# Kernel optimization log

Measured on AMD Instinct MI355X. Metric: run time of the kernel, lower is better.

Reference implementation:

```python
import jax, jax.numpy as jnp
import numpy as np

N = 50000       # nodes
E = 1_600_000   # edges (avg degree 32)
NFEAT = 256
NHID = 128
NCLASS = 128    # must equal NHID for the gated skip connection to type-check


def setup_inputs() -> dict:
    key = jax.random.key(0)
    ks = jax.random.split(key, 16)
    g = 0.02  # xavier gain used in the module
    inp = {
        "x": jax.random.normal(ks[0], (N, NFEAT), dtype=jnp.float32),
        "row": jax.random.randint(ks[1], (E,), 0, N, dtype=jnp.int32),
        "col": jax.random.randint(ks[2], (E,), 0, N, dtype=jnp.int32),
        # GatedSkipConnection params (shared across the three skip calls)
        "W_sc": jax.random.normal(ks[3], (NFEAT, NHID), dtype=jnp.float32) * 0.05,
        "W_ci": jax.random.normal(ks[4], (NHID, NHID), dtype=jnp.float32) * 0.05,
        "b_ci": jnp.zeros((NHID,), dtype=jnp.float32),
        "W_co": jax.random.normal(ks[5], (NHID, NHID), dtype=jnp.float32) * 0.05,
        "b_co": jnp.zeros((NHID,), dtype=jnp.float32),
        # GraphSAGE layer weights: [2*in, out], bias [1, out] (init to 0 per module)
        "W0": jax.random.normal(ks[6], (2 * NFEAT, NHID), dtype=jnp.float32) * g,
        "b0": jnp.zeros((1, NHID), dtype=jnp.float32),
        "W1": jax.random.normal(ks[7], (2 * NHID, NHID), dtype=jnp.float32) * g,
        "b1": jnp.zeros((1, NHID), dtype=jnp.float32),
        "W2": jax.random.normal(ks[8], (2 * NHID, NCLASS), dtype=jnp.float32) * g,
        "b2": jnp.zeros((1, NCLASS), dtype=jnp.float32),
        # fc0: Linear(nhid, nclass)
        "Wf": jax.random.normal(ks[9], (NHID, NCLASS), dtype=jnp.float32) * 0.05,
        "bf": jnp.zeros((NCLASS,), dtype=jnp.float32),
    }
    return inp


def _sage(x, row, col, inv_deg, W, b):
    # adj @ x : sum source features x[col] into destination rows `row`
    agg = jax.ops.segment_sum(x[col], row, num_segments=N)  # [N, d]
    agg = agg * inv_deg[:, None]                            # degree normalization
    support = jnp.concatenate([x, agg], axis=1)             # [N, 2d]
    return support @ W + b


def _gsc(in_x, out_x, W_sc, W_ci, b_ci, W_co, b_co):
    in_x = in_x @ W_sc if in_x.shape[1] != out_x.shape[1] else in_x
    z = jax.nn.sigmoid(in_x @ W_ci + b_ci + out_x @ W_co + b_co)
    return z * out_x + (1.0 - z) * in_x


def reference(x, row, col, W_sc, W_ci, b_ci, W_co, b_co,
              W0, b0, W1, b1, W2, b2, Wf, bf):
    deg = jax.ops.segment_sum(jnp.ones((E,), x.dtype), row, num_segments=N)
    inv_deg = 1.0 / jnp.maximum(deg, 1.0)  # guard isolated nodes

    residual = x
    o1 = _sage(x, row, col, inv_deg, W0, b0)
    o3 = jax.nn.relu(_gsc(residual, o1, W_sc, W_ci, b_ci, W_co, b_co))
    o4 = _sage(o3, row, col, inv_deg, W1, b1)
    o6 = jax.nn.relu(_gsc(residual, o4, W_sc, W_ci, b_ci, W_co, b_co))
    o7 = _sage(o6, row, col, inv_deg, W2, b2)
    o8 = _gsc(residual, o7, W_sc, W_ci, b_ci, W_co, b_co)
    return o8 @ Wf + bf
```

## Files before the change

### kernel.cpp

```cpp
#include <hip/hip_runtime.h>
#include <hip/hip_bf16.h>
#include <hip/hip_fp16.h>
#include <math.h>

#define NN 50000
#define EE 1600000
#define NFEAT 256
#define NHID 128
#define RNG 6250
#define NPASS 8
#define CPAD 16

typedef _Float16 f16;
typedef _Float16 f16x8 __attribute__((ext_vector_type(8)));
typedef _Float16 f16x4 __attribute__((ext_vector_type(4)));
typedef float f32x4 __attribute__((ext_vector_type(4)));

struct WPtrs {
    const float* s[10];
    f16* d[10];
};

__global__ __launch_bounds__(256) void k_prep(const float* __restrict__ x,
                                              f16* __restrict__ xh, int n4,
                                              int* __restrict__ cnt, int nz4,
                                              WPtrs wp, int wtotal,
                                              int zb0, int wb0, int wblocks) {
    int b = blockIdx.x;
    if (b < zb0) {
        int i = b * 256 + threadIdx.x;
        if (i < n4) {
            float4 v = reinterpret_cast<const float4*>(x)[i];
            f16x4 h = {(f16)v.x, (f16)v.y, (f16)v.z, (f16)v.w};
            reinterpret_cast<f16x4*>(xh)[i] = h;
        }
    } else if (b < wb0) {
        int i = (b - zb0) * 256 + threadIdx.x;
        if (i < nz4) reinterpret_cast<int4*>(cnt)[i] = make_int4(0, 0, 0, 0);
    } else {
        for (int idx = (b - wb0) * 256 + threadIdx.x; idx < wtotal;
             idx += wblocks * 256) {
            int wsel, rem, K;
            if (idx < 3 * 32768) { wsel = idx >> 15; rem = idx & 32767; K = 256; }
            else { int t = idx - 3 * 32768; wsel = 3 + (t >> 14); rem = t & 16383; K = 128; }
            int k = rem >> 7, c = rem & 127;
            wp.d[wsel][c * K + k] = (f16)wp.s[wsel][rem];
        }
    }
}

__global__ void k_slot(const int* __restrict__ row, int* __restrict__ cnt,
                       int* __restrict__ eslot, int e) {
    int i = blockIdx.x * 256 + threadIdx.x;
    if (i < e) eslot[i] = atomicAdd(&cnt[(size_t)row[i] * CPAD], 1);
}

__global__ void k_scan1(const int* __restrict__ cnt, int* __restrict__ bsum, int n) {
    __shared__ int s[256];
    int t = threadIdx.x;
    int i = blockIdx.x * 256 + t;
    s[t] = (i < n) ? cnt[(size_t)i * CPAD] : 0;
    __syncthreads();
    for (int off = 128; off > 0; off >>= 1) {
        if (t < off) s[t] += s[t + off];
        __syncthreads();
    }
    if (t == 0) bsum[blockIdx.x] = s[0];
}

__global__ void k_scan3(const int* __restrict__ cnt, const int* __restrict__ bsum,
                        int* __restrict__ rp, float* __restrict__ invd,
                        int n, int nb) {
    __shared__ int buf[2][256];
    __shared__ int bpre[2][256];
    int t = threadIdx.x;

    bpre[0][t] = (t < nb) ? bsum[t] : 0;
    __syncthreads();
    int bs = 0;
    for (int off = 1; off < 256; off <<= 1) {
        int v = bpre[bs][t];
        if (t >= off) v += bpre[bs][t - off];
        bpre[bs ^ 1][t] = v;
        bs ^= 1;
        __syncthreads();
    }
    int base = (blockIdx.x == 0) ? 0 : bpre[bs][blockIdx.x - 1];

    int i = blockIdx.x * 256 + t;
    int v = (i < n) ? cnt[(size_t)i * CPAD] : 0;
    buf[0][t] = v;
    __syncthreads();
    int sel = 0;
    for (int off = 1; off < 256; off <<= 1) {
        int x = buf[sel][t];
        if (t >= off) x += buf[sel][t - off];
        buf[sel ^ 1][t] = x;
        sel ^= 1;
        __syncthreads();
    }
    int incl = buf[sel][t];
    int excl = incl - v;
    if (i < n) {
        rp[i] = base + excl;
        invd[i] = 1.0f / fmaxf((float)v, 1.0f);
        if (i == n - 1) rp[n] = base + incl;
    }
}

__global__ void k_fill8(const int* __restrict__ row, const int* __restrict__ col,
                        const int* __restrict__ eslot, const int* __restrict__ rp,
                        int* __restrict__ ci, int e) {
    int i = blockIdx.x * 256 + threadIdx.x;
    if (i >= e) return;
    int r = row[i];
    int lo = blockIdx.y * RNG;
    if (r >= lo && r < lo + RNG) ci[rp[r] + eslot[i]] = col[i];
}

__global__ __launch_bounds__(256) void k_agg2h(const f16* __restrict__ P,
                                               const int* __restrict__ rp,
                                               const int* __restrict__ ci,
                                               const float* __restrict__ invd,
                                               const f16* __restrict__ T,
                                               f16* __restrict__ OUT, int n) {
    int node = blockIdx.x * 16 + (threadIdx.x >> 4);
    if (node >= n) return;
    int lane = threadIdx.x & 15;
    int s = rp[node], e = rp[node + 1];
    float acc[8];
#pragma unroll
    for (int q = 0; q < 8; ++q) acc[q] = 0.0f;
    int j = s;
    for (; j + 8 <= e; j += 8) {
        f16x8 v[8];
#pragma unroll
        for (int u = 0; u < 8; ++u)
            v[u] = *reinterpret_cast<const f16x8*>(P + (size_t)ci[j + u] * 128 + lane * 8);
#pragma unroll
        for (int q = 0; q < 8; ++q)
            acc[q] += (((float)v[0][q] + (float)v[1][q]) + ((float)v[2][q] + (float)v[3][q])) +
                      (((float)v[4][q] + (float)v[5][q]) + ((float)v[6][q] + (float)v[7][q]));
    }
    for (; j < e; ++j) {
        f16x8 v0 = *reinterpret_cast<const f16x8*>(P + (size_t)ci[j] * 128 + lane * 8);
#pragma unroll
        for (int q = 0; q < 8; ++q) acc[q] += (float)v0[q];
    }
    float scl = invd[node];
    f16x8 tv = *reinterpret_cast<const f16x8*>(T + (size_t)node * 128 + lane * 8);
    f16x8 o;
#pragma unroll
    for (int q = 0; q < 8; ++q) o[q] = (f16)((float)tv[q] + scl * acc[q]);
    *reinterpret_cast<f16x8*>(OUT + (size_t)node * 128 + lane * 8) = o;
}

#define LDSSTR 40

__device__ __forceinline__ void stage_A(const f16* __restrict__ A, f16* sA,
                                        int row0, int K, int kb, int tid, int n) {
    int r = tid >> 2, ch = tid & 3;
    int gr = row0 + r;
    uint4 v = make_uint4(0, 0, 0, 0);
    if (gr < n) v = *reinterpret_cast<const uint4*>(A + (size_t)gr * K + kb + ch * 8);
    *reinterpret_cast<uint4*>(sA + r * LDSSTR + ch * 8) = v;
}

__device__ __forceinline__ void stage_B(const f16* __restrict__ Wt, f16* sB,
                                        int K, int kb, int tid) {
#pragma unroll
    for (int i = 0; i < 2; ++i) {
        int idx = tid + i * 256;
        int c = idx >> 2, ch = idx & 3;
        uint4 v = *reinterpret_cast<const uint4*>(Wt + (size_t)c * K + kb + ch * 8);
        *reinterpret_cast<uint4*>(sB + c * LDSSTR + ch * 8) = v;
    }
}

template <int K, int NW, bool F32OUT>
__global__ __launch_bounds__(256) void k_mgemm(const f16* __restrict__ A,
                                               const f16* __restrict__ Wt0,
                                               const f16* __restrict__ Wt1,
                                               const f16* __restrict__ Wt2,
                                               const float* __restrict__ bias0,
                                               void* __restrict__ C0,
                                               void* __restrict__ C1,
                                               void* __restrict__ C2, int n) {
    __shared__ f16 sA[64 * LDSSTR];
    __shared__ f16 sB[128 * LDSSTR];

    const f16* Wt = Wt0;
    const float* bias = bias0;
    void* C = C0;
    if (NW > 1 && blockIdx.y == 1) { Wt = Wt1; bias = nullptr; C = C1; }
    if (NW > 2 && blockIdx.y == 2) { Wt = Wt2; bias = nullptr; C = C2; }

    const int tid = threadIdx.x;
    const int row0 = blockIdx.x * 64;
    const int wid = tid >> 6, l = tid & 63;
    const int wr = wid >> 1, wc = wid & 1;
    const int lr = l & 15, lk = (l >> 4) * 8;

    f32x4 acc[2][4];
#pragma unroll
    for (int m = 0; m < 2; ++m)
#pragma unroll
        for (int q = 0; q < 4; ++q) acc[m][q] = (f32x4){0.f, 0.f, 0.f, 0.f};

    for (int kt = 0; kt < K / 32; ++kt) {
        stage_A(A, sA, row0, K, kt * 32, tid, n);
        stage_B(Wt, sB, K, kt * 32, tid);
        __syncthreads();
        f16x8 aF[2], bF[4];
#pragma unroll
        for (int m = 0; m < 2; ++m)
            aF[m] = *reinterpret_cast<f16x8*>(sA + (wr * 32 + m * 16 + lr) * LDSSTR + lk);
#pragma unroll
        for (int q = 0; q < 4; ++q)
            bF[q] = *reinterpret_cast<f16x8*>(sB + (wc * 64 + q * 16 + lr) * LDSSTR + lk);
#pragma unroll
        for (int m = 0; m < 2; ++m)
#pragma unroll
            for (int q = 0; q < 4; ++q)
                acc[m][q] = __builtin_amdgcn_mfma_f32_16x16x32_f16(aF[m], bF[q],
                                                                   acc[m][q], 0, 0, 0);
        __syncthreads();
    }

    const int lr4 = (l >> 4) * 4;
#pragma unroll
    for (int m = 0; m < 2; ++m)
#pragma unroll
        for (int q = 0; q < 4; ++q) {
            int c = wc * 64 + q * 16 + (l & 15);
            float b = bias ? bias[c] : 0.0f;
#pragma unroll
            for (int reg = 0; reg < 4; ++reg) {
                int r = row0 + wr * 32 + m * 16 + lr4 + reg;
                if (r >= n) continue;
                float v = acc[m][q][reg] + b;
                if (F32OUT) ((float*)C)[(size_t)r * 128 + c] = v;
                else        ((f16*)C)[(size_t)r * 128 + c] = (f16)v;
            }
        }
}

template <int RELU>
__global__ __launch_bounds__(256) void k_ggemm(const f16* __restrict__ Asc,
                                               const f16* __restrict__ At0,
                                               const f16* __restrict__ Wci,
                                               const f16* __restrict__ Wco,
                                               const float* __restrict__ bci,
                                               const float* __restrict__ bco,
                                               f16* __restrict__ C, int n) {
    __shared__ f16 sA[64 * LDSSTR];
    __shared__ f16 sB[128 * LDSSTR];

    const int tid = threadIdx.x;
    const int row0 = blockIdx.x * 64;
    const int wid = tid >> 6, l = tid & 63;
    const int wr = wid >> 1, wc = wid & 1;
    const int lr = l & 15, lk = (l >> 4) * 8;

    f32x4 acc[2][4];
#pragma unroll
    for (int m = 0; m < 2; ++m)
#pragma unroll
        for (int q = 0; q < 4; ++q) acc[m][q] = (f32x4){0.f, 0.f, 0.f, 0.f};

    for (int kt = 0; kt < 8; ++kt) {
        const f16* A = (kt < 4) ? Asc : At0;
        const f16* Wt = (kt < 4) ? Wci : Wco;
        int kb = (kt & 3) * 32;
        stage_A(A, sA, row0, 128, kb, tid, n);
        stage_B(Wt, sB, 128, kb, tid);
        __syncthreads();
        f16x8 aF[2], bF[4];
#pragma unroll
        for (int m = 0; m < 2; ++m)
            aF[m] = *reinterpret_cast<f16x8*>(sA + (wr * 32 + m * 16 + lr) * LDSSTR + lk);
#pragma unroll
        for (int q = 0; q < 4; ++q)
            bF[q] = *reinterpret_cast<f16x8*>(sB + (wc * 64 + q * 16 + lr) * LDSSTR + lk);
#pragma unroll
        for (int m = 0; m < 2; ++m)
#pragma unroll
            for (int q = 0; q < 4; ++q)
                acc[m][q] = __builtin_amdgcn_mfma_f32_16x16x32_f16(aF[m], bF[q],
                                                                   acc[m][q], 0, 0, 0);
        __syncthreads();
    }

    const int lr4 = (l >> 4) * 4;
#pragma unroll
    for (int m = 0; m < 2; ++m)
#pragma unroll
        for (int q = 0; q < 4; ++q) {
            int c = wc * 64 + q * 16 + (l & 15);
            float b = bci[c] + bco[c];
#pragma unroll
            for (int reg = 0; reg < 4; ++reg) {
                int r = row0 + wr * 32 + m * 16 + lr4 + reg;
                if (r >= n) continue;
                float v = acc[m][q][reg] + b;
                float z = 1.0f / (1.0f + __expf(-v));
                float o = (float)At0[(size_t)r * 128 + c];
                float s = (float)Asc[(size_t)r * 128 + c];
                float outv = z * o + (1.0f - z) * s;
                if (RELU) outv = fmaxf(outv, 0.0f);
                C[(size_t)r * 128 + c] = (f16)outv;
            }
        }
}

extern "C" void kernel_launch(void* const* d_in, const int* in_sizes, int n_in,
                              void* d_out, int out_size, void* d_ws, size_t ws_size,
                              hipStream_t stream) {
    const float* x    = (const float*)d_in[0];
    const int*   row  = (const int*)d_in[1];
    const int*   col  = (const int*)d_in[2];
    const float* W_sc = (const float*)d_in[3];
    const float* W_ci = (const float*)d_in[4];
    const float* b_ci = (const float*)d_in[5];
    const float* W_co = (const float*)d_in[6];
    const float* b_co = (const float*)d_in[7];
    const float* W0   = (const float*)d_in[8];
    const float* b0   = (const float*)d_in[9];
    const float* W1   = (const float*)d_in[10];
    const float* b1   = (const float*)d_in[11];
    const float* W2   = (const float*)d_in[12];
    const float* b2   = (const float*)d_in[13];
    const float* Wf   = (const float*)d_in[14];
    const float* bf   = (const float*)d_in[15];
    float* out = (float*)d_out;

    char* p = (char*)d_ws;
    auto alloc = [&](size_t bytes) {
        char* q = p;
        p += (bytes + 255) & ~(size_t)255;
        return q;
    };
    int*   cnt   = (int*)alloc((size_t)NN * CPAD * 4);
    int*   rp    = (int*)alloc((NN + 1) * 4);
    int*   bsum  = (int*)alloc(256 * 4);
    float* invd  = (float*)alloc(NN * 4);
    int*   ci    = (int*)alloc(EE * 4);
    int*   eslot = (int*)alloc(EE * 4);
    f16*   x_h   = (f16*)alloc((size_t)NN * 256 * 2);
    f16*   sc_h  = (f16*)alloc((size_t)NN * 128 * 2);
    f16*   T_h   = (f16*)alloc((size_t)NN * 128 * 2);
    f16*   P_h   = (f16*)alloc((size_t)NN * 128 * 2);
    f16*   t0_h  = (f16*)alloc((size_t)NN * 128 * 2);
    f16*   t1_h  = (f16*)alloc((size_t)NN * 128 * 2);
    f16* W0t_t = (f16*)alloc(256 * 128 * 2);
    f16* W0b_t = (f16*)alloc(256 * 128 * 2);
    f16* Wsc_t = (f16*)alloc(256 * 128 * 2);
    f16* W1t_t = (f16*)alloc(128 * 128 * 2);
    f16* W1b_t = (f16*)alloc(128 * 128 * 2);
    f16* W2t_t = (f16*)alloc(128 * 128 * 2);
    f16* W2b_t = (f16*)alloc(128 * 128 * 2);
    f16* Wci_t = (f16*)alloc(128 * 128 * 2);
    f16* Wco_t = (f16*)alloc(128 * 128 * 2);
    f16* Wf_t  = (f16*)alloc(128 * 128 * 2);

    const int NB_N  = (NN + 255) / 256;
    const int NB_E  = (EE + 255) / 256;
    const int GB    = (NN + 63) / 64;
    const int AGG_B = (NN + 15) / 16;

    const int N4   = NN * 256 / 4;
    const int NZ4  = NN * CPAD / 4;
    const int ZB0  = (N4 + 255) / 256;
    const int WB0  = ZB0 + (NZ4 + 255) / 256;
    const int WBLK = 84;
    const int WTOT = 3 * 32768 + 7 * 16384;
    WPtrs wp;
    wp.s[0] = W0;             wp.d[0] = W0t_t;
    wp.s[1] = W0 + 256 * 128; wp.d[1] = W0b_t;
    wp.s[2] = W_sc;           wp.d[2] = Wsc_t;
    wp.s[3] = W1;             wp.d[3] = W1t_t;
    wp.s[4] = W1 + 128 * 128; wp.d[4] = W1b_t;
    wp.s[5] = W2;             wp.d[5] = W2t_t;
    wp.s[6] = W2 + 128 * 128; wp.d[6] = W2b_t;
    wp.s[7] = W_ci;           wp.d[7] = Wci_t;
    wp.s[8] = W_co;           wp.d[8] = Wco_t;
    wp.s[9] = Wf;             wp.d[9] = Wf_t;
    k_prep<<<WB0 + WBLK, 256, 0, stream>>>(x, x_h, N4, cnt, NZ4, wp, WTOT,
                                           ZB0, WB0, WBLK);

    k_slot<<<NB_E, 256, 0, stream>>>(row, cnt, eslot, EE);
    k_scan1<<<NB_N, 256, 0, stream>>>(cnt, bsum, NN);
    k_scan3<<<NB_N, 256, 0, stream>>>(cnt, bsum, rp, invd, NN, NB_N);
    k_fill8<<<dim3(NB_E, NPASS), 256, 0, stream>>>(row, col, eslot, rp, ci, EE);

    k_mgemm<256, 3, false><<<dim3(GB, 3), 256, 0, stream>>>(
        x_h, W0t_t, W0b_t, Wsc_t, b0, T_h, P_h, sc_h, NN);
    k_agg2h<<<AGG_B, 256, 0, stream>>>(P_h, rp, ci, invd, T_h, t0_h, NN);
    k_ggemm<1><<<GB, 256, 0, stream>>>(sc_h, t0_h, Wci_t, Wco_t,
                                       b_ci, b_co, t1_h, NN);

    k_mgemm<128, 2, false><<<dim3(GB, 2), 256, 0, stream>>>(
        t1_h, W1t_t, W1b_t, nullptr, b1, T_h, P_h, nullptr, NN);
    k_agg2h<<<AGG_B, 256, 0, stream>>>(P_h, rp, ci, invd, T_h, t0_h, NN);
    k_ggemm<1><<<GB, 256, 0, stream>>>(sc_h, t0_h, Wci_t, Wco_t,
                                       b_ci, b_co, t1_h, NN);

    k_mgemm<128, 2, false><<<dim3(GB, 2), 256, 0, stream>>>(
        t1_h, W2t_t, W2b_t, nullptr, b2, T_h, P_h, nullptr, NN);
    k_agg2h<<<AGG_B, 256, 0, stream>>>(P_h, rp, ci, invd, T_h, t0_h, NN);
    k_ggemm<0><<<GB, 256, 0, stream>>>(sc_h, t0_h, Wci_t, Wco_t,
                                       b_ci, b_co, t1_h, NN);

    k_mgemm<128, 1, true><<<GB, 256, 0, stream>>>(
        t1_h, Wf_t, nullptr, nullptr, bf, out, nullptr, nullptr, NN);
}
```

Measured before the change: 541.8 us.

## Fuse gated skip with following SAGE GEMM, pack edge slot with row

Merges the gated-skip GEMM+sigmoid blend with the next layer's T/P projection GEMM (or the final classifier) into one kernel. The intermediate activation stays in LDS instead of going through global memory, and three launches are removed. Weights are read straight from global/L2 rather than staged in LDS. Edge slot and row are packed into one int, which assumes slot < 32768 and row < 65536, and the fill runs in 4 row-range passes instead of 8.

```diff
diff --git a/kernel.cpp b/kernel.cpp
--- a/kernel.cpp
+++ b/kernel.cpp
@@ -7,8 +7,8 @@
 #define EE 1600000
 #define NFEAT 256
 #define NHID 128
-#define RNG 6250
-#define NPASS 8
+#define RNG 12500
+#define NPASS 4
 #define CPAD 16
 
 typedef _Float16 f16;
@@ -50,9 +50,13 @@
 }
 
 __global__ void k_slot(const int* __restrict__ row, int* __restrict__ cnt,
-                       int* __restrict__ eslot, int e) {
+                       int* __restrict__ epack, int e) {
     int i = blockIdx.x * 256 + threadIdx.x;
-    if (i < e) eslot[i] = atomicAdd(&cnt[(size_t)row[i] * CPAD], 1);
+    if (i < e) {
+        int r = row[i];
+        int s = atomicAdd(&cnt[(size_t)r * CPAD], 1);
+        epack[i] = (s << 16) | r;
+    }
 }
 
 __global__ void k_scan1(const int* __restrict__ cnt, int* __restrict__ bsum, int n) {
@@ -108,14 +112,14 @@
     }
 }
 
-__global__ void k_fill8(const int* __restrict__ row, const int* __restrict__ col,
-                        const int* __restrict__ eslot, const int* __restrict__ rp,
-                        int* __restrict__ ci, int e) {
+__global__ void k_fill(const int* __restrict__ epack, const int* __restrict__ col,
+                       const int* __restrict__ rp, int* __restrict__ ci, int e) {
     int i = blockIdx.x * 256 + threadIdx.x;
     if (i >= e) return;
-    int r = row[i];
+    int pk = epack[i];
+    int r = pk & 0xFFFF;
     int lo = blockIdx.y * RNG;
-    if (r >= lo && r < lo + RNG) ci[rp[r] + eslot[i]] = col[i];
+    if (r >= lo && r < lo + RNG) ci[rp[r] + (pk >> 16)] = col[i];
 }
 
 __global__ __launch_bounds__(256) void k_agg2h(const f16* __restrict__ P,
@@ -245,70 +249,150 @@
         }
 }
 
-template <int RELU>
-__global__ __launch_bounds__(256) void k_ggemm(const f16* __restrict__ Asc,
+#define FSTR 136
+
+template <int RELU, bool CLS>
+__global__ __launch_bounds__(256) void k_fused(const f16* __restrict__ Asc,
                                                const f16* __restrict__ At0,
                                                const f16* __restrict__ Wci,
                                                const f16* __restrict__ Wco,
+                                               const f16* __restrict__ WtT,
+                                               const f16* __restrict__ WtP,
                                                const float* __restrict__ bci,
                                                const float* __restrict__ bco,
-                                               f16* __restrict__ C, int n) {
-    __shared__ f16 sA[64 * LDSSTR];
-    __shared__ f16 sB[128 * LDSSTR];
+                                               const float* __restrict__ bias2,
+                                               f16* __restrict__ To,
+                                               f16* __restrict__ Po,
+                                               float* __restrict__ Fo, int n) {
+    __shared__ f16 lsc[64 * FSTR];
+    __shared__ f16 lt0[64 * FSTR];
+    __shared__ f16 lt1[64 * FSTR];
 
     const int tid = threadIdx.x;
     const int row0 = blockIdx.x * 64;
     const int wid = tid >> 6, l = tid & 63;
     const int wr = wid >> 1, wc = wid & 1;
     const int lr = l & 15, lk = (l >> 4) * 8;
-
-    f32x4 acc[2][4];
-#pragma unroll
-    for (int m = 0; m < 2; ++m)
-#pragma unroll
-        for (int q = 0; q < 4; ++q) acc[m][q] = (f32x4){0.f, 0.f, 0.f, 0.f};
-
-    for (int kt = 0; kt < 8; ++kt) {
-        const f16* A = (kt < 4) ? Asc : At0;
-        const f16* Wt = (kt < 4) ? Wci : Wco;
-        int kb = (kt & 3) * 32;
-        stage_A(A, sA, row0, 128, kb, tid, n);
-        stage_B(Wt, sB, 128, kb, tid);
-        __syncthreads();
-        f16x8 aF[2], bF[4];
+    const int lr4 = (l >> 4) * 4;
+
+#pragma unroll
+    for (int i = 0; i < 4; ++i) {
+        int idx = tid + i * 256;
+        int r = idx >> 4, ch = idx & 15;
+        int gr = row0 + r;
+        uint4 vs = make_uint4(0, 0, 0, 0), vt = make_uint4(0, 0, 0, 0);
+        if (gr < n) {
+            vs = *reinterpret_cast<const uint4*>(Asc + (size_t)gr * 128 + ch * 8);
+            vt = *reinterpret_cast<const uint4*>(At0 + (size_t)gr * 128 + ch * 8);
+        }
+        *reinterpret_cast<uint4*>(lsc + r * FSTR + ch * 8) = vs;
+        *reinterpret_cast<uint4*>(lt0 + r * FSTR + ch * 8) = vt;
+    }
+    __syncthreads();
+
+    f32x4 accG[2][4];
+#pragma unroll
+    for (int m = 0; m < 2; ++m)
+#pragma unroll
+        for (int q = 0; q < 4; ++q) accG[m][q] = (f32x4){0.f, 0.f, 0.f, 0.f};
+
+#pragma unroll
+    for (int kt = 0; kt < 4; ++kt) {
+        f16x8 aS[2], aT[2], bC[4], bO[4];
+#pragma unroll
+        for (int m = 0; m < 2; ++m) {
+            int rr = (wr * 32 + m * 16 + lr) * FSTR + kt * 32 + lk;
+            aS[m] = *reinterpret_cast<const f16x8*>(lsc + rr);
+            aT[m] = *reinterpret_cast<const f16x8*>(lt0 + rr);
+        }
+#pragma unroll
+        for (int q = 0; q < 4; ++q) {
+            int c = wc * 64 + q * 16 + lr;
+            bC[q] = *reinterpret_cast<const f16x8*>(Wci + (size_t)c * 128 + kt * 32 + lk);
+            bO[q] = *reinterpret_cast<const f16x8*>(Wco + (size_t)c * 128 + kt * 32 + lk);
+        }
 #pragma unroll
         for (int m = 0; m < 2; ++m)
-            aF[m] = *reinterpret_cast<f16x8*>(sA + (wr * 32 + m * 16 + lr) * LDSSTR + lk);
-#pragma unroll
-        for (int q = 0; q < 4; ++q)
-            bF[q] = *reinterpret_cast<f16x8*>(sB + (wc * 64 + q * 16 + lr) * LDSSTR + lk);
+#pragma unroll
+            for (int q = 0; q < 4; ++q) {
+                accG[m][q] = __builtin_amdgcn_mfma_f32_16x16x32_f16(aS[m], bC[q],
+                                                                    accG[m][q], 0, 0, 0);
+                accG[m][q] = __builtin_amdgcn_mfma_f32_16x16x32_f16(aT[m], bO[q],
+                                                                    accG[m][q], 0, 0, 0);
+            }
+    }
+
+#pragma unroll
+    for (int m = 0; m < 2; ++m)
+#pragma unroll
+        for (int q = 0; q < 4; ++q) {
+            int c = wc * 64 + q * 16 + (l & 15);
+            float bb = bci[c] + bco[c];
+#pragma unroll
+            for (int reg = 0; reg < 4; ++reg) {
+                int lrow = wr * 32 + m * 16 + lr4 + reg;
+                float v = accG[m][q][reg] + bb;
+                float z = 1.0f / (1.0f + __expf(-v));
+                float o = (float)lt0[lrow * FSTR + c];
+                float s = (float)lsc[lrow * FSTR + c];
+                float t1v = z * o + (1.0f - z) * s;
+                if (RELU) t1v = fmaxf(t1v, 0.0f);
+                lt1[lrow * FSTR + c] = (f16)t1v;
+            }
+        }
+    __syncthreads();
+
+    f32x4 accT[2][4], accP[2][4];
+#pragma unroll
+    for (int m = 0; m < 2; ++m)
+#pragma unroll
+        for (int q = 0; q < 4; ++q) {
+            accT[m][q] = (f32x4){0.f, 0.f, 0.f, 0.f};
+            accP[m][q] = (f32x4){0.f, 0.f, 0.f, 0.f};
+        }
+
+#pragma unroll
+    for (int kt = 0; kt < 4; ++kt) {
+        f16x8 aF[2], bT[4], bP[4];
 #pragma unroll
         for (int m = 0; m < 2; ++m)
-#pragma unroll
-            for (int q = 0; q < 4; ++q)
-                acc[m][q] = __builtin_amdgcn_mfma_f32_16x16x32_f16(aF[m], bF[q],
-                                                                   acc[m][q], 0, 0, 0);
-        __syncthreads();
-    }
-
-    const int lr4 = (l >> 4) * 4;
+            aF[m] = *reinterpret_cast<const f16x8*>(
+                lt1 + (wr * 32 + m * 16 + lr) * FSTR + kt * 32 + lk);
+#pragma unroll
+        for (int q = 0; q < 4; ++q) {
+            int c = wc * 64 + q * 16 + lr;
+            bT[q] = *reinterpret_cast<const f16x8*>(WtT + (size_t)c * 128 + kt * 32 + lk);
+            if (!CLS)
+                bP[q] = *reinterpret_cast<const f16x8*>(WtP + (size_t)c * 128 + kt * 32 + lk);
+        }
+#pragma unroll
+        for (int m = 0; m < 2; ++m)
+#pragma unroll
+            for (int q = 0; q < 4; ++q) {
+                accT[m][q] = __builtin_amdgcn_mfma_f32_16x16x32_f16(aF[m], bT[q],
+                                                                    accT[m][q], 0, 0, 0);
+                if (!CLS)
+                    accP[m][q] = __builtin_amdgcn_mfma_f32_16x16x32_f16(aF[m], bP[q],
+                                                                        accP[m][q], 0, 0, 0);
+            }
+    }
+
 #pragma unroll
     for (int m = 0; m < 2; ++m)
 #pragma unroll
         for (int q = 0; q < 4; ++q) {
             int c = wc * 64 + q * 16 + (l & 15);
-            float b = bci[c] + bco[c];
+            float b = bias2[c];
 #pragma unroll
             for (int reg = 0; reg < 4; ++reg) {
                 int r = row0 + wr * 32 + m * 16 + lr4 + reg;
                 if (r >= n) continue;
-                float v = acc[m][q][reg] + b;
-                float z = 1.0f / (1.0f + __expf(-v));
-                float o = (float)At0[(size_t)r * 128 + c];
-                float s = (float)Asc[(size_t)r * 128 + c];
-                float outv = z * o + (1.0f - z) * s;
-                if (RELU) outv = fmaxf(outv, 0.0f);
-                C[(size_t)r * 128 + c] = (f16)outv;
+                if (CLS) {
+                    Fo[(size_t)r * 128 + c] = accT[m][q][reg] + b;
+                } else {
+                    To[(size_t)r * 128 + c] = (f16)(accT[m][q][reg] + b);
+                    Po[(size_t)r * 128 + c] = (f16)accP[m][q][reg];
+                }
             }
         }
 }
@@ -345,13 +429,12 @@
     int*   bsum  = (int*)alloc(256 * 4);
     float* invd  = (float*)alloc(NN * 4);
     int*   ci    = (int*)alloc(EE * 4);
-    int*   eslot = (int*)alloc(EE * 4);
+    int*   epack = (int*)alloc(EE * 4);
     f16*   x_h   = (f16*)alloc((size_t)NN * 256 * 2);
     f16*   sc_h  = (f16*)alloc((size_t)NN * 128 * 2);
     f16*   T_h   = (f16*)alloc((size_t)NN * 128 * 2);
     f16*   P_h   = (f16*)alloc((size_t)NN * 128 * 2);
     f16*   t0_h  = (f16*)alloc((size_t)NN * 128 * 2);
-    f16*   t1_h  = (f16*)alloc((size_t)NN * 128 * 2);
     f16* W0t_t = (f16*)alloc(256 * 128 * 2);
     f16* W0b_t = (f16*)alloc(256 * 128 * 2);
     f16* Wsc_t = (f16*)alloc(256 * 128 * 2);
@@ -388,29 +471,26 @@
     k_prep<<<WB0 + WBLK, 256, 0, stream>>>(x, x_h, N4, cnt, NZ4, wp, WTOT,
                                            ZB0, WB0, WBLK);
 
-    k_slot<<<NB_E, 256, 0, stream>>>(row, cnt, eslot, EE);
+    k_slot<<<NB_E, 256, 0, stream>>>(row, cnt, epack, EE);
     k_scan1<<<NB_N, 256, 0, stream>>>(cnt, bsum, NN);
     k_scan3<<<NB_N, 256, 0, stream>>>(cnt, bsum, rp, invd, NN, NB_N);
-    k_fill8<<<dim3(NB_E, NPASS), 256, 0, stream>>>(row, col, eslot, rp, ci, EE);
+    k_fill<<<dim3(NB_E, NPASS), 256, 0, stream>>>(epack, col, rp, ci, EE);
 
     k_mgemm<256, 3, false><<<dim3(GB, 3), 256, 0, stream>>>(
         x_h, W0t_t, W0b_t, Wsc_t, b0, T_h, P_h, sc_h, NN);
     k_agg2h<<<AGG_B, 256, 0, stream>>>(P_h, rp, ci, invd, T_h, t0_h, NN);
-    k_ggemm<1><<<GB, 256, 0, stream>>>(sc_h, t0_h, Wci_t, Wco_t,
-                                       b_ci, b_co, t1_h, NN);
-
-    k_mgemm<128, 2, false><<<dim3(GB, 2), 256, 0, stream>>>(
-        t1_h, W1t_t, W1b_t, nullptr, b1, T_h, P_h, nullptr, NN);
+
+    k_fused<1, false><<<GB, 256, 0, stream>>>(
+        sc_h, t0_h, Wci_t, Wco_t, W1t_t, W1b_t, b_ci, b_co, b1,
+        T_h, P_h, nullptr, NN);
     k_agg2h<<<AGG_B, 256, 0, stream>>>(P_h, rp, ci, invd, T_h, t0_h, NN);
-    k_ggemm<1><<<GB, 256, 0, stream>>>(sc_h, t0_h, Wci_t, Wco_t,
-                                       b_ci, b_co, t1_h, NN);
-
-    k_mgemm<128, 2, false><<<dim3(GB, 2), 256, 0, stream>>>(
-        t1_h, W2t_t, W2b_t, nullptr, b2, T_h, P_h, nullptr, NN);
+
+    k_fused<1, false><<<GB, 256, 0, stream>>>(
+        sc_h, t0_h, Wci_t, Wco_t, W2t_t, W2b_t, b_ci, b_co, b2,
+        T_h, P_h, nullptr, NN);
     k_agg2h<<<AGG_B, 256, 0, stream>>>(P_h, rp, ci, invd, T_h, t0_h, NN);
-    k_ggemm<0><<<GB, 256, 0, stream>>>(sc_h, t0_h, Wci_t, Wco_t,
-                                       b_ci, b_co, t1_h, NN);
-
-    k_mgemm<128, 1, true><<<GB, 256, 0, stream>>>(
-        t1_h, Wf_t, nullptr, nullptr, bf, out, nullptr, nullptr, NN);
-}
+
+    k_fused<0, true><<<GB, 256, 0, stream>>>(
+        sc_h, t0_h, Wci_t, Wco_t, Wf_t, nullptr, b_ci, b_co, bf,
+        nullptr, nullptr, out, NN);
+}
```

Measured after the change: 544.7 us. Within noise of the previous version (+0.5%).
